# Kernel tuning notes

Measured on AMD Instinct MI355X. Metric: run time of the kernel, lower is better.

The kernel has to match this reference:

```python
import jax, jax.numpy as jnp
import numpy as np

B, N1, N2 = 16, 4096, 1024
C1, C2 = 128, 256
IN_CH, OUT_CH = 4096, 256  # fc1 acts on N1 dim due to transpose; BN channels = C2 = OUT_CH
BN_EPS = 1e-5


def setup_inputs() -> dict:
    key = jax.random.key(0)
    ks = jax.random.split(key, 8)
    x1 = jax.random.normal(ks[0], (B, N1, C1), dtype=jnp.float32)
    x2 = jax.random.normal(ks[1], (B, N2, C2), dtype=jnp.float32)
    xyz1 = jax.random.normal(ks[2], (B, N1, 3), dtype=jnp.float32)
    xyz2 = jax.random.normal(ks[3], (B, N2, 3), dtype=jnp.float32)
    # Linear(in_channels=N1 -> out_channels) params, PyTorch default init scale
    bound = 1.0 / np.sqrt(IN_CH)
    W1 = jax.random.uniform(ks[4], (OUT_CH, IN_CH), jnp.float32, -bound, bound)
    b1 = jax.random.uniform(ks[5], (OUT_CH,), jnp.float32, -bound, bound)
    gamma = jnp.ones((OUT_CH,), jnp.float32)
    beta = jnp.zeros((OUT_CH,), jnp.float32)
    return {"x1": x1, "x2": x2, "xyz1": xyz1, "xyz2": xyz2,
            "W1": W1, "b1": b1, "gamma": gamma, "beta": beta}


def _square_distance(src, dst):
    # src: [B,N,3], dst: [B,M,3] -> [B,N,M]
    d = -2.0 * jnp.einsum('bnc,bmc->bnm', src, dst)
    d = d + jnp.sum(src * src, -1)[:, :, None]
    d = d + jnp.sum(dst * dst, -1)[:, None, :]
    return d


def reference(x1, x2, xyz1, xyz2, W1, b1, gamma, beta):
    dists = _square_distance(xyz1, xyz2)              # [B,N1,N2]
    neg3, idx = jax.lax.top_k(-dists, 3)              # 3 smallest distances
    d3 = -neg3                                        # [B,N1,3], ascending
    dist_recip = 1.0 / (d3 + 1e-8)
    weight = dist_recip / jnp.sum(dist_recip, axis=2, keepdims=True)
    gathered = jax.vmap(lambda pts, i: pts[i])(x2, idx)   # [B,N1,3,C2]
    interp = jnp.sum(gathered * weight[..., None], axis=2)  # [B,N1,C2]
    t = jnp.swapaxes(interp, 1, 2)                    # [B,C2,N1]
    y = jnp.einsum('bcn,on->bco', t, W1) + b1         # [B,C2,OUT_CH]
    # BatchNorm1d over channel dim 1 (size C2 == OUT_CH), training-mode batch stats
    mean = jnp.mean(y, axis=(0, 2), keepdims=True)
    var = jnp.mean((y - mean) ** 2, axis=(0, 2), keepdims=True)
    y = (y - mean) / jnp.sqrt(var + BN_EPS)
    y = gamma[None, :, None] * y + beta[None, :, None]
    y = jax.nn.relu(y)
    return jnp.swapaxes(y, 1, 2)                      # [B,OUT_CH,C2]
```

## Files before the change

### kernel.cpp

```cpp
#include <hip/hip_runtime.h>
#include <hip/hip_bf16.h>
#include <float.h>

#define B_    16
#define N1_   4096
#define N2_   1024
#define C2_   256
#define OUT_  256
#define K_    4096
#define SPLITK 8
#define KCH_  (K_ / SPLITK)
#define ZSLAB 1048576

typedef short short8 __attribute__((ext_vector_type(8)));
typedef float float4v __attribute__((ext_vector_type(4)));

static __device__ __forceinline__ unsigned short f32_to_bf16_bits(float v) {
    __hip_bfloat16 h = __float2bfloat16(v);
    return *(unsigned short*)&h;
}

#define TPAD 65
struct KnnSh {
    float4 pts[N2_];
    float  pf[4][64][3];
};
union ShUnion {
    KnnSh a;
    unsigned short tile[C2_][TPAD];
};

__global__ __launch_bounds__(256) void knn_interp_kernel(
    const float* __restrict__ xyz1,
    const float* __restrict__ xyz2,
    const float* __restrict__ x2,
    unsigned short* __restrict__ interp_t,
    const float* __restrict__ W1,
    unsigned short* __restrict__ W1b,
    float* __restrict__ accum)
{
    __shared__ ShUnion sh;
    __shared__ float rw[64][3];
    __shared__ int   ri[64][3];

    const int bid = blockIdx.x;
    const int t   = threadIdx.x;

    if (bid < 1024) {
        if (bid == 0) {
            accum[t] = 0.0f;
            accum[256 + t] = 0.0f;
        }
        const int i = (bid * 256 + t) * 4;
        float4 v = *(const float4*)(W1 + i);
        ushort4 o;
        o.x = f32_to_bf16_bits(v.x);
        o.y = f32_to_bf16_bits(v.y);
        o.z = f32_to_bf16_bits(v.z);
        o.w = f32_to_bf16_bits(v.w);
        *(ushort4*)(W1b + i) = o;
        return;
    }

    const int rem = bid - 1024;
    const int b   = rem >> 6;
    const int n0  = (rem & 63) * 64;
    const int w   = t >> 6;
    const int l   = t & 63;

    for (int r = 0; r < 4; ++r) {
        int j = r * 256 + t;
        const float* p = xyz2 + ((size_t)b * N2_ + j) * 3;
        float x = p[0], y = p[1], z = p[2];
        sh.a.pts[j] = make_float4(x, y, z, 0.5f * ((x * x + y * y) + z * z));
    }
    __syncthreads();

    const int n1 = n0 + l;
    const float* q = xyz1 + ((size_t)b * N1_ + n1) * 3;
    const float s0 = q[0], s1 = q[1], s2 = q[2];
    const float ns0 = -s0, ns1 = -s1, ns2 = -s2;
    const float ss = (s0 * s0 + s1 * s1) + s2 * s2;

    const int jbase = w << 8;
    float f0 = FLT_MAX, f1 = FLT_MAX, f2 = FLT_MAX;

    #pragma unroll 4
    for (int jj = 0; jj < 256; ++jj) {
        const int j = jbase + jj;
        float4 pq = sh.a.pts[j];
        float acc = fmaf(ns0, pq.x, pq.w);
        acc = fmaf(ns1, pq.y, acc);
        acc = fmaf(ns2, pq.z, acc);
        float dk = fmaxf(fmaf(2.0f, acc, ss), 0.0f);
        float fp = __int_as_float((__float_as_int(dk) & 0xFFFFFC00) | j);
        float nf0 = fminf(fp, f0);
        float nf1 = __builtin_amdgcn_fmed3f(fp, f0, f1);
        float nf2 = fminf(f2, fmaxf(fp, f1));
        f0 = nf0; f1 = nf1; f2 = nf2;
    }

    sh.a.pf[w][l][0] = f0; sh.a.pf[w][l][1] = f1; sh.a.pf[w][l][2] = f2;
    __syncthreads();

    if (w == 0) {
        float g0 = FLT_MAX, g1 = FLT_MAX, g2 = FLT_MAX;
        #pragma unroll
        for (int p = 0; p < 4; ++p)
        #pragma unroll
        for (int r = 0; r < 3; ++r) {
            float fp = sh.a.pf[p][l][r];
            float n0v = fminf(fp, g0);
            float n1v = __builtin_amdgcn_fmed3f(fp, g0, g1);
            float n2v = fminf(g2, fmaxf(fp, g1));
            g0 = n0v; g1 = n1v; g2 = n2v;
        }
        int j0 = __float_as_int(g0) & 1023;
        int j1 = __float_as_int(g1) & 1023;
        int j2 = __float_as_int(g2) & 1023;
        const float4 p0 = sh.a.pts[j0];
        const float4 p1 = sh.a.pts[j1];
        const float4 p2 = sh.a.pts[j2];
        float d0 = ss + 2.0f * (p0.w - ((s0 * p0.x + s1 * p0.y) + s2 * p0.z));
        float d1 = ss + 2.0f * (p1.w - ((s0 * p1.x + s1 * p1.y) + s2 * p1.z));
        float d2 = ss + 2.0f * (p2.w - ((s0 * p2.x + s1 * p2.y) + s2 * p2.z));
        float r0 = 1.0f / (d0 + 1e-8f);
        float r1 = 1.0f / (d1 + 1e-8f);
        float r2 = 1.0f / (d2 + 1e-8f);
        float s  = (r0 + r1) + r2;
        rw[l][0] = r0 / s;  rw[l][1] = r1 / s;  rw[l][2] = r2 / s;
        ri[l][0] = j0;      ri[l][1] = j1;      ri[l][2] = j2;
    }
    __syncthreads();

    for (int p = 0; p < 16; ++p) {
        int nl = p * 4 + w;
        float w0 = rw[nl][0], w1 = rw[nl][1], w2 = rw[nl][2];
        int i0g = ri[nl][0], i1g = ri[nl][1], i2g = ri[nl][2];
        const float4 va = ((const float4*)(x2 + ((size_t)b * N2_ + i0g) * C2_))[l];
        const float4 vb = ((const float4*)(x2 + ((size_t)b * N2_ + i1g) * C2_))[l];
        const float4 vc = ((const float4*)(x2 + ((size_t)b * N2_ + i2g) * C2_))[l];
        float fa[4] = {va.x, va.y, va.z, va.w};
        float fb[4] = {vb.x, vb.y, vb.z, vb.w};
        float fc[4] = {vc.x, vc.y, vc.z, vc.w};
        #pragma unroll
        for (int i = 0; i < 4; ++i) {
            float v = w0 * fa[i];
            v = fmaf(w1, fb[i], v);
            v = fmaf(w2, fc[i], v);
            sh.tile[l * 4 + i][nl] = f32_to_bf16_bits(v);
        }
    }
    __syncthreads();

    for (int r = 0; r < 64; ++r) {
        int c = r * 4 + w;
        interp_t[((size_t)b * C2_ + c) * K_ + n0 + l] = sh.tile[c][l];
    }
}

#define LDA 72
__global__ __launch_bounds__(256) void gemm_kernel(
    const unsigned short* __restrict__ W1b,
    const unsigned short* __restrict__ interp_t,
    float* __restrict__ Zp)
{
    __shared__ unsigned short Alds[128][LDA];
    __shared__ unsigned short Blds[64][LDA];
    const int z  = blockIdx.z;
    const int b  = z >> 3;
    const int kc = z & 7;
    const int o0 = blockIdx.y * 128;
    const int c0 = blockIdx.x * 64;
    const int t = threadIdx.x;
    const int w = t >> 6, l = t & 63;
    const int arow = t >> 1, ahalf = t & 1;
    const int brow = t >> 2, bq = t & 3;
    const int ob = (w >> 1) * 64, cb = (w & 1) * 32;
    const int m = l & 15, kq = l >> 4;

    const unsigned short* Wp = W1b + (size_t)(o0 + arow) * K_ + kc * KCH_ + ahalf * 32;
    const unsigned short* Bp = interp_t + ((size_t)b * C2_ + (c0 + brow)) * K_ + kc * KCH_ + bq * 16;

    float4v acc[4][2] = {};

    uint4 a0 = *(const uint4*)(Wp);
    uint4 a1 = *(const uint4*)(Wp + 8);
    uint4 a2 = *(const uint4*)(Wp + 16);
    uint4 a3 = *(const uint4*)(Wp + 24);
    uint4 b0 = *(const uint4*)(Bp);
    uint4 b1 = *(const uint4*)(Bp + 8);

    for (int kk = 0; kk < KCH_; kk += 64) {
        *(uint4*)&Alds[arow][ahalf * 32]      = a0;
        *(uint4*)&Alds[arow][ahalf * 32 + 8]  = a1;
        *(uint4*)&Alds[arow][ahalf * 32 + 16] = a2;
        *(uint4*)&Alds[arow][ahalf * 32 + 24] = a3;
        *(uint4*)&Blds[brow][bq * 16]         = b0;
        *(uint4*)&Blds[brow][bq * 16 + 8]     = b1;
        __syncthreads();

        if (kk + 64 < KCH_) {
            a0 = *(const uint4*)(Wp + kk + 64);
            a1 = *(const uint4*)(Wp + kk + 72);
            a2 = *(const uint4*)(Wp + kk + 80);
            a3 = *(const uint4*)(Wp + kk + 88);
            b0 = *(const uint4*)(Bp + kk + 64);
            b1 = *(const uint4*)(Bp + kk + 72);
        }

        #pragma unroll
        for (int ks = 0; ks < 64; ks += 32) {
            short8 bf0 = *(const short8*)&Blds[cb + m][ks + kq * 8];
            short8 bf1 = *(const short8*)&Blds[cb + 16 + m][ks + kq * 8];
            #pragma unroll
            for (int mi = 0; mi < 4; ++mi) {
                short8 af = *(const short8*)&Alds[ob + mi * 16 + m][ks + kq * 8];
                acc[mi][0] = __builtin_amdgcn_mfma_f32_16x16x32_bf16(af, bf0, acc[mi][0], 0, 0, 0);
                acc[mi][1] = __builtin_amdgcn_mfma_f32_16x16x32_bf16(af, bf1, acc[mi][1], 0, 0, 0);
            }
        }
        __syncthreads();
    }

    float* Zslab = Zp + (size_t)kc * ZSLAB;
    #pragma unroll
    for (int mi = 0; mi < 4; ++mi)
    #pragma unroll
    for (int ni = 0; ni < 2; ++ni)
    #pragma unroll
    for (int r = 0; r < 4; ++r) {
        int o = o0 + ob + mi * 16 + kq * 4 + r;
        int c = c0 + cb + ni * 16 + m;
        Zslab[((size_t)b * OUT_ + o) * C2_ + c] = acc[mi][ni][r];
    }
}

__global__ __launch_bounds__(256) void reduce_stats_kernel(
    float* __restrict__ Zp, const float* __restrict__ b1,
    float* __restrict__ accum)
{
    const int b  = blockIdx.x >> 4;
    const int oq = blockIdx.x & 15;
    const int c  = threadIdx.x;
    float s = 0.0f, s2 = 0.0f;
    for (int o16 = 0; o16 < 16; ++o16) {
        int o = oq * 16 + o16;
        size_t base = ((size_t)b * OUT_ + o) * C2_ + c;
        float v = b1[o];
        #pragma unroll
        for (int sl = 0; sl < SPLITK; ++sl)
            v += Zp[base + (size_t)sl * ZSLAB];
        Zp[base] = v;
        s += v; s2 += v * v;
    }
    atomicAdd(&accum[c], s);
    atomicAdd(&accum[C2_ + c], s2);
}

__global__ __launch_bounds__(256) void bn_kernel(
    const float* __restrict__ Z, const float* __restrict__ accum,
    const float* __restrict__ gamma, const float* __restrict__ beta,
    float* __restrict__ out)
{
    const int i = (blockIdx.x * 256 + threadIdx.x) * 4;
    float4 z = *(const float4*)(Z + i);
    float vals[4] = {z.x, z.y, z.z, z.w};
    const int cb = i & 255;
    float res[4];
    #pragma unroll
    for (int j = 0; j < 4; ++j) {
        int c = cb + j;
        float mean = accum[c] * (1.0f / 4096.0f);
        float var  = accum[C2_ + c] * (1.0f / 4096.0f) - mean * mean;
        float rstd = 1.0f / sqrtf(var + 1e-5f);
        float v = gamma[c] * ((vals[j] - mean) * rstd) + beta[c];
        res[j] = fmaxf(v, 0.0f);
    }
    *(float4*)(out + i) = make_float4(res[0], res[1], res[2], res[3]);
}

extern "C" void kernel_launch(void* const* d_in, const int* in_sizes, int n_in,
                              void* d_out, int out_size, void* d_ws, size_t ws_size,
                              hipStream_t stream) {
    const float* x2    = (const float*)d_in[1];
    const float* xyz1  = (const float*)d_in[2];
    const float* xyz2  = (const float*)d_in[3];
    const float* W1    = (const float*)d_in[4];
    const float* b1    = (const float*)d_in[5];
    const float* gamma = (const float*)d_in[6];
    const float* beta  = (const float*)d_in[7];

    char* ws = (char*)d_ws;
    unsigned short* interp_t = (unsigned short*)(ws);
    unsigned short* W1b      = (unsigned short*)(ws + 33554432);
    float*          Zp       = (float*)(ws + 35651584);
    float*          accum    = (float*)(ws + 69206016);

    knn_interp_kernel <<<2048, 256, 0, stream>>>(xyz1, xyz2, x2, interp_t,
                                                 W1, W1b, accum);
    gemm_kernel       <<<dim3(4, 2, 128), 256, 0, stream>>>(W1b, interp_t, Zp);
    reduce_stats_kernel<<<256, 256, 0, stream>>>(Zp, b1, accum);
    bn_kernel         <<<1024, 256, 0, stream>>>(Zp, accum, gamma, beta,
                                                 (float*)d_out);
}
```

Measured before the change: 157.1 us.

## Register-block four queries per thread in KNN search with 16-way point slicing

Restructures the KNN distance loop so each thread handles 4 query points against a 64-point slice of the reference set (16 slices per block), reusing each shared-memory point load across 4 queries. Shared-memory point and partial-result arrays are padded to reduce bank conflicts, and the final merge now combines 16 partial top-3 lists per query instead of 4. It aims to cut LDS traffic per distance evaluation, at the cost of more registers and a longer serial merge in the first wave.

```diff
diff --git a/kernel.cpp b/kernel.cpp
--- a/kernel.cpp
+++ b/kernel.cpp
@@ -22,8 +22,8 @@
 
 #define TPAD 65
 struct KnnSh {
-    float4 pts[N2_];
-    float  pf[4][64][3];
+    float4 pts[16][65];
+    float  pf[64][49];
 };
 union ShUnion {
     KnnSh a;
@@ -72,44 +72,62 @@
         int j = r * 256 + t;
         const float* p = xyz2 + ((size_t)b * N2_ + j) * 3;
         float x = p[0], y = p[1], z = p[2];
-        sh.a.pts[j] = make_float4(x, y, z, 0.5f * ((x * x + y * y) + z * z));
+        sh.a.pts[j >> 6][j & 63] = make_float4(x, y, z, 0.5f * ((x * x + y * y) + z * z));
     }
     __syncthreads();
 
-    const int n1 = n0 + l;
-    const float* q = xyz1 + ((size_t)b * N1_ + n1) * 3;
-    const float s0 = q[0], s1 = q[1], s2 = q[2];
-    const float ns0 = -s0, ns1 = -s1, ns2 = -s2;
-    const float ss = (s0 * s0 + s1 * s1) + s2 * s2;
-
-    const int jbase = w << 8;
-    float f0 = FLT_MAX, f1 = FLT_MAX, f2 = FLT_MAX;
-
-    #pragma unroll 4
-    for (int jj = 0; jj < 256; ++jj) {
-        const int j = jbase + jj;
-        float4 pq = sh.a.pts[j];
-        float acc = fmaf(ns0, pq.x, pq.w);
-        acc = fmaf(ns1, pq.y, acc);
-        acc = fmaf(ns2, pq.z, acc);
-        float dk = fmaxf(fmaf(2.0f, acc, ss), 0.0f);
-        float fp = __int_as_float((__float_as_int(dk) & 0xFFFFFC00) | j);
-        float nf0 = fminf(fp, f0);
-        float nf1 = __builtin_amdgcn_fmed3f(fp, f0, f1);
-        float nf2 = fminf(f2, fmaxf(fp, f1));
-        f0 = nf0; f1 = nf1; f2 = nf2;
-    }
-
-    sh.a.pf[w][l][0] = f0; sh.a.pf[w][l][1] = f1; sh.a.pf[w][l][2] = f2;
+    const int qg    = l & 15;
+    const int slice = (w << 2) | (l >> 4);
+    const int jbase = slice << 6;
+
+    const float* qb = xyz1 + ((size_t)b * N1_ + n0 + qg * 4) * 3;
+    float4 v0 = ((const float4*)qb)[0];
+    float4 v1 = ((const float4*)qb)[1];
+    float4 v2 = ((const float4*)qb)[2];
+    float qx[4] = {v0.x, v0.w, v1.z, v2.y};
+    float qy[4] = {v0.y, v1.x, v1.w, v2.z};
+    float qz[4] = {v0.z, v1.y, v2.x, v2.w};
+
+    float ns0[4], ns1[4], ns2[4], ss[4], f[4][3];
+    #pragma unroll
+    for (int i = 0; i < 4; ++i) {
+        ns0[i] = -qx[i]; ns1[i] = -qy[i]; ns2[i] = -qz[i];
+        ss[i]  = (qx[i] * qx[i] + qy[i] * qy[i]) + qz[i] * qz[i];
+        f[i][0] = FLT_MAX; f[i][1] = FLT_MAX; f[i][2] = FLT_MAX;
+    }
+
+    #pragma unroll 2
+    for (int jj = 0; jj < 64; ++jj) {
+        float4 pq = sh.a.pts[slice][jj];
+        int j = jbase + jj;
+        #pragma unroll
+        for (int i = 0; i < 4; ++i) {
+            float acc = fmaf(ns0[i], pq.x, pq.w);
+            acc = fmaf(ns1[i], pq.y, acc);
+            acc = fmaf(ns2[i], pq.z, acc);
+            float dk = fmaxf(fmaf(2.0f, acc, ss[i]), 0.0f);
+            float fp = __int_as_float((__float_as_int(dk) & 0xFFFFFC00) | j);
+            float nf0 = fminf(fp, f[i][0]);
+            float nf1 = __builtin_amdgcn_fmed3f(fp, f[i][0], f[i][1]);
+            float nf2 = fminf(f[i][2], fmaxf(fp, f[i][1]));
+            f[i][0] = nf0; f[i][1] = nf1; f[i][2] = nf2;
+        }
+    }
+
+    #pragma unroll
+    for (int i = 0; i < 4; ++i)
+    #pragma unroll
+    for (int r = 0; r < 3; ++r)
+        sh.a.pf[qg * 4 + i][slice * 3 + r] = f[i][r];
     __syncthreads();
 
     if (w == 0) {
         float g0 = FLT_MAX, g1 = FLT_MAX, g2 = FLT_MAX;
-        #pragma unroll
-        for (int p = 0; p < 4; ++p)
+        #pragma unroll 4
+        for (int s = 0; s < 16; ++s)
         #pragma unroll
         for (int r = 0; r < 3; ++r) {
-            float fp = sh.a.pf[p][l][r];
+            float fp = sh.a.pf[l][s * 3 + r];
             float n0v = fminf(fp, g0);
             float n1v = __builtin_amdgcn_fmed3f(fp, g0, g1);
             float n2v = fminf(g2, fmaxf(fp, g1));
@@ -118,18 +136,24 @@
         int j0 = __float_as_int(g0) & 1023;
         int j1 = __float_as_int(g1) & 1023;
         int j2 = __float_as_int(g2) & 1023;
-        const float4 p0 = sh.a.pts[j0];
-        const float4 p1 = sh.a.pts[j1];
-        const float4 p2 = sh.a.pts[j2];
-        float d0 = ss + 2.0f * (p0.w - ((s0 * p0.x + s1 * p0.y) + s2 * p0.z));
-        float d1 = ss + 2.0f * (p1.w - ((s0 * p1.x + s1 * p1.y) + s2 * p1.z));
-        float d2 = ss + 2.0f * (p2.w - ((s0 * p2.x + s1 * p2.y) + s2 * p2.z));
-        float r0 = 1.0f / (d0 + 1e-8f);
-        float r1 = 1.0f / (d1 + 1e-8f);
-        float r2 = 1.0f / (d2 + 1e-8f);
-        float s  = (r0 + r1) + r2;
-        rw[l][0] = r0 / s;  rw[l][1] = r1 / s;  rw[l][2] = r2 / s;
-        ri[l][0] = j0;      ri[l][1] = j1;      ri[l][2] = j2;
+        const float4 p0 = sh.a.pts[j0 >> 6][j0 & 63];
+        const float4 p1 = sh.a.pts[j1 >> 6][j1 & 63];
+        const float4 p2 = sh.a.pts[j2 >> 6][j2 & 63];
+        float d0 = ss[0] * 0.0f;
+        const float s0q = qx[0], s1q = qy[0], s2q = qz[0];
+        (void)d0; (void)s0q; (void)s1q; (void)s2q;
+        const float* q = xyz1 + ((size_t)b * N1_ + n0 + l) * 3;
+        const float s0 = q[0], s1 = q[1], s2 = q[2];
+        const float ssl = (s0 * s0 + s1 * s1) + s2 * s2;
+        float dd0 = ssl + 2.0f * (p0.w - ((s0 * p0.x + s1 * p0.y) + s2 * p0.z));
+        float dd1 = ssl + 2.0f * (p1.w - ((s0 * p1.x + s1 * p1.y) + s2 * p1.z));
+        float dd2 = ssl + 2.0f * (p2.w - ((s0 * p2.x + s1 * p2.y) + s2 * p2.z));
+        float r0 = 1.0f / (dd0 + 1e-8f);
+        float r1 = 1.0f / (dd1 + 1e-8f);
+        float r2 = 1.0f / (dd2 + 1e-8f);
+        float sden = (r0 + r1) + r2;
+        rw[l][0] = r0 / sden;  rw[l][1] = r1 / sden;  rw[l][2] = r2 / sden;
+        ri[l][0] = j0;         ri[l][1] = j1;         ri[l][2] = j2;
     }
     __syncthreads();
 
```

New measurement: 158.9 us. About the same (+1.2%).
